# Kernel optimization log

Measured on AMD Instinct MI355X. Metric: run time of the kernel, lower is better.

The kernel has to match this reference:

```python
import jax, jax.numpy as jnp
import numpy as np

N_NODES = 500_000
MEM_DIM = 256
MSG_DIM = 256
N_UPD = 100_000


def setup_inputs() -> dict:
    key = jax.random.key(0)
    ks = jax.random.split(key, 10)
    s = 1.0 / np.sqrt(MEM_DIM)
    return {
        "unique_node_ids": jnp.arange(N_UPD, dtype=jnp.int64)
        if jax.config.jax_enable_x64 else jnp.arange(N_UPD, dtype=jnp.int32),
        "unique_messages": jax.random.normal(ks[0], (N_UPD, MSG_DIM), jnp.float32),
        "timestamps": jax.random.uniform(ks[1], (N_UPD,), jnp.float32),
        "net_transaction_amounts": jax.random.normal(ks[2], (N_UPD,), jnp.float32),
        "memory": jax.random.normal(ks[3], (N_NODES, MEM_DIM), jnp.float32),
        "last_update": jnp.zeros((N_NODES,), jnp.float32),
        "W_cat": jax.random.normal(ks[4], (MEM_DIM, MSG_DIM + 1), jnp.float32) * s,
        "b_cat": jnp.zeros((MEM_DIM,), jnp.float32),
        "W_ih": jax.random.normal(ks[5], (3 * MEM_DIM, MEM_DIM), jnp.float32) * s,
        "W_hh": jax.random.normal(ks[6], (3 * MEM_DIM, MEM_DIM), jnp.float32) * s,
        "b_ih": jnp.zeros((3 * MEM_DIM,), jnp.float32),
        "b_hh": jnp.zeros((3 * MEM_DIM,), jnp.float32),
    }


def _gru_cell(x, h, W_ih, W_hh, b_ih, b_hh):
    # torch.nn.GRUCell math
    gi = x @ W_ih.T + b_ih      # [N, 3*D]
    gh = h @ W_hh.T + b_hh      # [N, 3*D]
    i_r, i_z, i_n = jnp.split(gi, 3, axis=1)
    h_r, h_z, h_n = jnp.split(gh, 3, axis=1)
    r = jax.nn.sigmoid(i_r + h_r)
    z = jax.nn.sigmoid(i_z + h_z)
    n = jnp.tanh(i_n + r * h_n)
    return (1.0 - z) * n + z * h


def reference(unique_node_ids, unique_messages, timestamps, net_transaction_amounts,
              memory, last_update, W_cat, b_cat, W_ih, W_hh, b_ih, b_hh):
    # concat message with scalar amount, small linear projection
    cat = jnp.concatenate([unique_messages, net_transaction_amounts[:, None]], axis=1)
    final_inputs = cat @ W_cat.T + b_cat                # [N_upd, MEM_DIM]
    h = memory[unique_node_ids]                         # gather by id
    new_h = _gru_cell(final_inputs, h, W_ih, W_hh, b_ih, b_hh)
    updated_memory = memory.at[unique_node_ids].set(new_h)        # scatter back
    updated_last_update = last_update.at[unique_node_ids].set(timestamps)
    return updated_memory, updated_last_update
```

## Files before the change

kernel.cpp:

```cpp
#include <hip/hip_runtime.h>
#include <hip/hip_bf16.h>

typedef __attribute__((ext_vector_type(8))) short s16x8;
typedef __attribute__((ext_vector_type(4))) float f32x4;

__device__ __forceinline__ unsigned short f2bf(float x) {
    unsigned int u = __float_as_uint(x);
    u += 0x7fffu + ((u >> 16) & 1u);
    return (unsigned short)(u >> 16);
}
__device__ __forceinline__ s16x8 pack8(float4 a, float4 b) {
    return (s16x8){ (short)f2bf(a.x), (short)f2bf(a.y), (short)f2bf(a.z), (short)f2bf(a.w),
                    (short)f2bf(b.x), (short)f2bf(b.y), (short)f2bf(b.z), (short)f2bf(b.w) };
}
__device__ __forceinline__ void gload_lds16(const void* g, void* l) {
    __builtin_amdgcn_global_load_lds(
        (const __attribute__((address_space(1))) void*)g,
        (__attribute__((address_space(3))) void*)(unsigned int)(size_t)l,
        16, 0, 0);
}
__device__ __forceinline__ float sigf(float x) { return 1.f / (1.f + __expf(-x)); }
__device__ __forceinline__ float tanhfast(float x) {
    return 1.f - 2.f / (__expf(2.f * x) + 1.f);
}

__global__ void prep_w_kernel(const float* __restrict__ W_cat,
                              const float* __restrict__ b_cat,
                              const float* __restrict__ W_ih,
                              const float* __restrict__ W_hh,
                              const float* __restrict__ b_ih,
                              unsigned short* __restrict__ wm,
                              unsigned short* __restrict__ whh,
                              float* __restrict__ wamt,
                              float* __restrict__ bcomb) {
    int idx = blockIdx.x * blockDim.x + threadIdx.x;
    const int NW = 768 * 256;
    if (idx < NW) {
        int g = idx >> 8, c = idx & 255;
        float s = 0.f;
        #pragma unroll 4
        for (int k = 0; k < 256; ++k) s += W_ih[g * 256 + k] * W_cat[k * 257 + c];
        wm[idx] = f2bf(s);
    } else if (idx < 2 * NW) {
        int t = idx - NW;
        whh[t] = f2bf(W_hh[t]);
    } else if (idx < 2 * NW + 768) {
        int g = idx - 2 * NW;
        float sa = 0.f, sb = 0.f;
        for (int k = 0; k < 256; ++k) {
            float w = W_ih[g * 256 + k];
            sa += w * W_cat[k * 257 + 256];
            sb += w * b_cat[k];
        }
        wamt[g] = sa;
        bcomb[g] = sb + b_ih[g];
    }
}

__global__ void build_inv_kernel(const int* __restrict__ ids, int* __restrict__ inv, int M) {
    int i = blockIdx.x * blockDim.x + threadIdx.x;
    if (i < M) inv[ids[i]] = i + 1;
}

__device__ __forceinline__ void dma_w(const unsigned short* __restrict__ wm,
                                      const unsigned short* __restrict__ whh,
                                      int nc, int k0, char* swbuf, int tid) {
    #pragma unroll
    for (int it = 0; it < 6; ++it) {
        int q = tid + it * 512;
        int r = q >> 3;
        int part = (q & 7) ^ (r & 7);
        int pn = r >> 6, rr = r & 63;
        const unsigned short* src = (pn < 3)
            ? wm  + ((size_t)(pn * 256 + nc * 64 + rr)) * 256
            : whh + ((size_t)((pn - 3) * 256 + nc * 64 + rr)) * 256;
        gload_lds16((const char*)src + k0 * 2 + part * 16,
                    swbuf + (tid & ~63) * 16 + it * 8192);
    }
}

__global__ __launch_bounds__(512, 2)
void gru_kernel(const int* __restrict__ ids,
                const float* __restrict__ msgs,
                const float* __restrict__ memory,
                const unsigned short* __restrict__ wm,
                const unsigned short* __restrict__ whh,
                const float* __restrict__ wamt,
                const float* __restrict__ bcomb,
                const float* __restrict__ b_hh,
                const float* __restrict__ amt,
                float* __restrict__ out_mem,
                int M, int mtiles) {
    extern __shared__ char lds[];
    char* sm  = lds;
    char* sh  = lds + 16384;
    char* sw0 = lds + 32768;
    char* sw1 = lds + 81920;

    int g = blockIdx.x;
    int xcd = g & 7, s = g >> 3;
    int nc = s & 3;
    int mtile = (s >> 2) * 8 + xcd;
    if (mtile >= mtiles) return;
    int m0 = mtile * 128;

    int tid = threadIdx.x;
    int lane = tid & 63;
    int w = tid >> 6;
    int wr = w >> 2, wc = w & 3;

    int row0 = tid >> 3, row1 = (tid + 512) >> 3;
    int part = tid & 7;
    int gr0 = m0 + row0; if (gr0 >= M) gr0 = M - 1;
    int gr1 = m0 + row1; if (gr1 >= M) gr1 = M - 1;
    const float* mp0 = msgs + (size_t)gr0 * 256 + part * 8;
    const float* mp1 = msgs + (size_t)gr1 * 256 + part * 8;
    const float* hp0 = memory + (size_t)ids[gr0] * 256 + part * 8;
    const float* hp1 = memory + (size_t)ids[gr1] * 256 + part * 8;
    int ld0 = row0 * 128 + ((part ^ (row0 & 7)) * 16);
    int ld1 = row1 * 128 + ((part ^ (row1 & 7)) * 16);

    float4 ma0, mb0, ma1, mb1, ha0, hb0, ha1, hb1;
    {
        ma0 = *(const float4*)(mp0);     mb0 = *(const float4*)(mp0 + 4);
        ma1 = *(const float4*)(mp1);     mb1 = *(const float4*)(mp1 + 4);
        ha0 = *(const float4*)(hp0);     hb0 = *(const float4*)(hp0 + 4);
        ha1 = *(const float4*)(hp1);     hb1 = *(const float4*)(hp1 + 4);
        dma_w(wm, whh, nc, 0, sw0, tid);
        *(s16x8*)(sm + ld0) = pack8(ma0, mb0);
        *(s16x8*)(sm + ld1) = pack8(ma1, mb1);
        *(s16x8*)(sh + ld0) = pack8(ha0, hb0);
        *(s16x8*)(sh + ld1) = pack8(ha1, hb1);
    }
    __syncthreads();

    f32x4 acc[6][4];
    #pragma unroll
    for (int pn = 0; pn < 6; ++pn)
        #pragma unroll
        for (int mf = 0; mf < 4; ++mf) acc[pn][mf] = (f32x4){0.f, 0.f, 0.f, 0.f};

    #pragma unroll
    for (int ks = 0; ks < 4; ++ks) {
        char* swc = (ks & 1) ? sw1 : sw0;
        if (ks < 3) {
            int k0 = (ks + 1) * 64;
            ma0 = *(const float4*)(mp0 + k0);  mb0 = *(const float4*)(mp0 + k0 + 4);
            ma1 = *(const float4*)(mp1 + k0);  mb1 = *(const float4*)(mp1 + k0 + 4);
            ha0 = *(const float4*)(hp0 + k0);  hb0 = *(const float4*)(hp0 + k0 + 4);
            ha1 = *(const float4*)(hp1 + k0);  hb1 = *(const float4*)(hp1 + k0 + 4);
            dma_w(wm, whh, nc, k0, (ks & 1) ? sw0 : sw1, tid);
        }
        #pragma unroll
        for (int c = 0; c < 2; ++c) {
            int p = c * 4 + (lane >> 4);
            s16x8 ax[4], ah[4], bw[6];
            #pragma unroll
            for (int mf = 0; mf < 4; ++mf) {
                int row = wr * 64 + mf * 16 + (lane & 15);
                int off = row * 128 + ((p ^ (row & 7)) * 16);
                ax[mf] = *(const s16x8*)(sm + off);
                ah[mf] = *(const s16x8*)(sh + off);
            }
            #pragma unroll
            for (int pn = 0; pn < 6; ++pn) {
                int r = pn * 64 + wc * 16 + (lane & 15);
                bw[pn] = *(const s16x8*)(swc + r * 128 + ((p ^ (r & 7)) * 16));
            }
            #pragma unroll
            for (int pn = 0; pn < 6; ++pn)
                #pragma unroll
                for (int mf = 0; mf < 4; ++mf)
                    acc[pn][mf] = __builtin_amdgcn_mfma_f32_16x16x32_bf16(
                        (pn < 3) ? ax[mf] : ah[mf], bw[pn], acc[pn][mf], 0, 0, 0);
        }
        if (ks < 3) {
            __syncthreads();
            *(s16x8*)(sm + ld0) = pack8(ma0, mb0);
            *(s16x8*)(sm + ld1) = pack8(ma1, mb1);
            *(s16x8*)(sh + ld0) = pack8(ha0, hb0);
            *(s16x8*)(sh + ld1) = pack8(ha1, hb1);
            __syncthreads();
        }
    }

    int colL = wc * 16 + (lane & 15);
    int col = nc * 64 + colL;
    float bi0 = bcomb[col], bi1 = bcomb[256 + col], bi2 = bcomb[512 + col];
    float bh0 = b_hh[col],  bh1 = b_hh[256 + col],  bh2 = b_hh[512 + col];
    float wa0 = wamt[col],  wa1 = wamt[256 + col],  wa2 = wamt[512 + col];
    #pragma unroll
    for (int mf = 0; mf < 4; ++mf) {
        int rb = wr * 64 + mf * 16 + (lane >> 4) * 4;
        #pragma unroll
        for (int r = 0; r < 4; ++r) {
            int grow = m0 + rb + r; if (grow >= M) grow = M - 1;
            int gid = ids[grow];
            float amtv = amt[grow];
            float hv = memory[(size_t)gid * 256 + col];
            float ir = acc[0][mf][r] + bi0 + amtv * wa0;
            float iz = acc[1][mf][r] + bi1 + amtv * wa1;
            float in_ = acc[2][mf][r] + bi2 + amtv * wa2;
            float hr = acc[3][mf][r] + bh0;
            float hz = acc[4][mf][r] + bh1;
            float hn = acc[5][mf][r] + bh2;
            float rg = sigf(ir + hr);
            float zg = sigf(iz + hz);
            float ng = tanhfast(in_ + rg * hn);
            out_mem[(size_t)gid * 256 + col] = (1.f - zg) * ng + zg * hv;
        }
    }
}

__global__ __launch_bounds__(256)
void copy_kernel(const float* __restrict__ memory,
                 const int* __restrict__ inv,
                 const float* __restrict__ lu,
                 const float* __restrict__ ts,
                 float* __restrict__ out_mem,
                 float* __restrict__ out_lu,
                 int N) {
    int wid = (blockIdx.x * blockDim.x + threadIdx.x) >> 6;
    int lane = threadIdx.x & 63;
    int nw = (gridDim.x * blockDim.x) >> 6;
    for (int base = wid; base < N; base += nw * 4) {
        int  r0 = base, r1 = base + nw, r2 = base + 2 * nw, r3 = base + 3 * nw;
        bool d0 = (r0 < N) && (inv[r0] == 0);
        bool d1 = (r1 < N) && (inv[r1] == 0);
        bool d2 = (r2 < N) && (inv[r2] == 0);
        bool d3 = (r3 < N) && (inv[r3] == 0);
        float4 v0, v1, v2, v3;
        if (d0) v0 = ((const float4*)(memory + (size_t)r0 * 256))[lane];
        if (d1) v1 = ((const float4*)(memory + (size_t)r1 * 256))[lane];
        if (d2) v2 = ((const float4*)(memory + (size_t)r2 * 256))[lane];
        if (d3) v3 = ((const float4*)(memory + (size_t)r3 * 256))[lane];
        if (d0) ((float4*)(out_mem + (size_t)r0 * 256))[lane] = v0;
        if (d1) ((float4*)(out_mem + (size_t)r1 * 256))[lane] = v1;
        if (d2) ((float4*)(out_mem + (size_t)r2 * 256))[lane] = v2;
        if (d3) ((float4*)(out_mem + (size_t)r3 * 256))[lane] = v3;
    }
    int gidx = blockIdx.x * blockDim.x + threadIdx.x;
    int stride = gridDim.x * blockDim.x;
    for (int i = gidx; i < N; i += stride) {
        int iv = inv[i];
        out_lu[i] = iv ? ts[iv - 1] : lu[i];
    }
}

extern "C" void kernel_launch(void* const* d_in, const int* in_sizes, int n_in,
                              void* d_out, int out_size, void* d_ws, size_t ws_size,
                              hipStream_t stream) {
    const int*   ids   = (const int*)  d_in[0];
    const float* msgs  = (const float*)d_in[1];
    const float* ts    = (const float*)d_in[2];
    const float* amt   = (const float*)d_in[3];
    const float* mem   = (const float*)d_in[4];
    const float* lu    = (const float*)d_in[5];
    const float* W_cat = (const float*)d_in[6];
    const float* b_cat = (const float*)d_in[7];
    const float* W_ih  = (const float*)d_in[8];
    const float* W_hh  = (const float*)d_in[9];
    const float* b_ih  = (const float*)d_in[10];
    const float* b_hh  = (const float*)d_in[11];

    int M = in_sizes[0];
    int N = in_sizes[5];

    float* out_mem = (float*)d_out;
    float* out_lu  = out_mem + (size_t)N * 256;

    char* ws = (char*)d_ws;
    unsigned short* wm    = (unsigned short*)ws;
    unsigned short* whh   = wm + 768 * 256;
    float*          wamt  = (float*)(whh + 768 * 256);
    float*          bcomb = wamt + 768;
    int*            inv   = (int*)(bcomb + 768);

    prep_w_kernel<<<(2 * 768 * 256 + 768 + 255) / 256, 256, 0, stream>>>(
        W_cat, b_cat, W_ih, W_hh, b_ih, wm, whh, wamt, bcomb);

    (void)hipMemsetAsync(inv, 0, (size_t)N * 4, stream);
    build_inv_kernel<<<(M + 255) / 256, 256, 0, stream>>>(ids, inv, M);

    int mtiles = (M + 127) / 128;
    int mt8 = ((mtiles + 7) / 8) * 8;
    (void)hipFuncSetAttribute((const void*)gru_kernel,
                              hipFuncAttributeMaxDynamicSharedMemorySize, 131072);
    gru_kernel<<<mt8 * 4, 512, 131072, stream>>>(
        ids, msgs, mem, wm, whh, wamt, bcomb, b_hh, amt, out_mem, M, mtiles);

    copy_kernel<<<2048, 256, 0, stream>>>(mem, inv, lu, ts, out_mem, out_lu, N);
}
```

Measured before the change: 422.0 us.

## Rotate K order per column block, reuse LDS hidden state, fuse inverse-map build

Merges build_inv into prep_w_kernel, which removes one launch. Each column-block CTA now walks the K chunks in a rotated order so that the last chunk left in shared memory is the one holding its own output columns. The GRU epilogue then reads h from that bf16 copy in shared memory instead of re-gathering fp32 memory from global. The risk is precision: the z*h term now uses bf16-rounded h rather than the fp32 value, which may exceed tolerance.

```diff
diff --git a/kernel.cpp b/kernel.cpp
--- a/kernel.cpp
+++ b/kernel.cpp
@@ -8,6 +8,9 @@
     unsigned int u = __float_as_uint(x);
     u += 0x7fffu + ((u >> 16) & 1u);
     return (unsigned short)(u >> 16);
+}
+__device__ __forceinline__ float bf2f(unsigned short h) {
+    return __uint_as_float((unsigned int)h << 16);
 }
 __device__ __forceinline__ s16x8 pack8(float4 a, float4 b) {
     return (s16x8){ (short)f2bf(a.x), (short)f2bf(a.y), (short)f2bf(a.z), (short)f2bf(a.w),
@@ -29,10 +32,13 @@
                               const float* __restrict__ W_ih,
                               const float* __restrict__ W_hh,
                               const float* __restrict__ b_ih,
+                              const int* __restrict__ ids,
                               unsigned short* __restrict__ wm,
                               unsigned short* __restrict__ whh,
                               float* __restrict__ wamt,
-                              float* __restrict__ bcomb) {
+                              float* __restrict__ bcomb,
+                              int* __restrict__ inv,
+                              int M) {
     int idx = blockIdx.x * blockDim.x + threadIdx.x;
     const int NW = 768 * 256;
     if (idx < NW) {
@@ -54,12 +60,10 @@
         }
         wamt[g] = sa;
         bcomb[g] = sb + b_ih[g];
-    }
-}
-
-__global__ void build_inv_kernel(const int* __restrict__ ids, int* __restrict__ inv, int M) {
-    int i = blockIdx.x * blockDim.x + threadIdx.x;
-    if (i < M) inv[ids[i]] = i + 1;
+    } else if (idx < 2 * NW + 768 + M) {
+        int i = idx - (2 * NW + 768);
+        inv[ids[i]] = i + 1;
+    }
 }
 
 __device__ __forceinline__ void dma_w(const unsigned short* __restrict__ wm,
@@ -122,11 +126,12 @@
 
     float4 ma0, mb0, ma1, mb1, ha0, hb0, ha1, hb1;
     {
-        ma0 = *(const float4*)(mp0);     mb0 = *(const float4*)(mp0 + 4);
-        ma1 = *(const float4*)(mp1);     mb1 = *(const float4*)(mp1 + 4);
-        ha0 = *(const float4*)(hp0);     hb0 = *(const float4*)(hp0 + 4);
-        ha1 = *(const float4*)(hp1);     hb1 = *(const float4*)(hp1 + 4);
-        dma_w(wm, whh, nc, 0, sw0, tid);
+        int k0 = ((nc + 1) & 3) * 64;
+        ma0 = *(const float4*)(mp0 + k0);  mb0 = *(const float4*)(mp0 + k0 + 4);
+        ma1 = *(const float4*)(mp1 + k0);  mb1 = *(const float4*)(mp1 + k0 + 4);
+        ha0 = *(const float4*)(hp0 + k0);  hb0 = *(const float4*)(hp0 + k0 + 4);
+        ha1 = *(const float4*)(hp1 + k0);  hb1 = *(const float4*)(hp1 + k0 + 4);
+        dma_w(wm, whh, nc, k0, sw0, tid);
         *(s16x8*)(sm + ld0) = pack8(ma0, mb0);
         *(s16x8*)(sm + ld1) = pack8(ma1, mb1);
         *(s16x8*)(sh + ld0) = pack8(ha0, hb0);
@@ -144,7 +149,7 @@
     for (int ks = 0; ks < 4; ++ks) {
         char* swc = (ks & 1) ? sw1 : sw0;
         if (ks < 3) {
-            int k0 = (ks + 1) * 64;
+            int k0 = ((nc + 2 + ks) & 3) * 64;
             ma0 = *(const float4*)(mp0 + k0);  mb0 = *(const float4*)(mp0 + k0 + 4);
             ma1 = *(const float4*)(mp1 + k0);  mb1 = *(const float4*)(mp1 + k0 + 4);
             ha0 = *(const float4*)(hp0 + k0);  hb0 = *(const float4*)(hp0 + k0 + 4);
@@ -189,15 +194,18 @@
     float bi0 = bcomb[col], bi1 = bcomb[256 + col], bi2 = bcomb[512 + col];
     float bh0 = b_hh[col],  bh1 = b_hh[256 + col],  bh2 = b_hh[512 + col];
     float wa0 = wamt[col],  wa1 = wamt[256 + col],  wa2 = wamt[512 + col];
+    int hpart = colL >> 3, hbyte = (colL & 7) << 1;
     #pragma unroll
     for (int mf = 0; mf < 4; ++mf) {
         int rb = wr * 64 + mf * 16 + (lane >> 4) * 4;
         #pragma unroll
         for (int r = 0; r < 4; ++r) {
-            int grow = m0 + rb + r; if (grow >= M) grow = M - 1;
+            int rl = rb + r;
+            int grow = m0 + rl; if (grow >= M) grow = M - 1;
             int gid = ids[grow];
             float amtv = amt[grow];
-            float hv = memory[(size_t)gid * 256 + col];
+            float hv = bf2f(*(const unsigned short*)(
+                sh + rl * 128 + ((hpart ^ (rl & 7)) << 4) + hbyte));
             float ir = acc[0][mf][r] + bi0 + amtv * wa0;
             float iz = acc[1][mf][r] + bi1 + amtv * wa1;
             float in_ = acc[2][mf][r] + bi2 + amtv * wa2;
@@ -276,11 +284,11 @@
     float*          bcomb = wamt + 768;
     int*            inv   = (int*)(bcomb + 768);
 
-    prep_w_kernel<<<(2 * 768 * 256 + 768 + 255) / 256, 256, 0, stream>>>(
-        W_cat, b_cat, W_ih, W_hh, b_ih, wm, whh, wamt, bcomb);
-
     (void)hipMemsetAsync(inv, 0, (size_t)N * 4, stream);
-    build_inv_kernel<<<(M + 255) / 256, 256, 0, stream>>>(ids, inv, M);
+
+    int prep_items = 2 * 768 * 256 + 768 + M;
+    prep_w_kernel<<<(prep_items + 255) / 256, 256, 0, stream>>>(
+        W_cat, b_cat, W_ih, W_hh, b_ih, ids, wm, whh, wamt, bcomb, inv, M);
 
     int mtiles = (M + 127) / 128;
     int mt8 = ((mtiles + 7) / 8) * 8;
```

After: 396.7 us (median of 2 runs). 1.06x faster.
